# Kernel optimization log

Hardware: AMD Instinct MI355X
Metric: run time of the kernel (lower is better)

## Reference

```python
import jax, jax.numpy as jnp
import numpy as np

N = 128                      # mesh size (must be even)
IL_MMI = 0.05                # insersion_loss_MMI
IMB = 0.005                  # imbalance_MMI
IL_X = 0.02                  # insersion_loss_Crossing
CT = 0.01                    # cross_talk_Crossing
TWO_PI = 6.283185307179586


def _build_constants():
    aM = np.sqrt(1.0 - IL_MMI)
    # 2x2 MMI block (even pairing (0,1),(2,3),...)
    B_mmi = aM * np.array([[np.sqrt(0.5 + IMB), 1j * np.sqrt(0.5 - IMB)],
                           [1j * np.sqrt(0.5 - IMB), np.sqrt(0.5 + IMB)]], dtype=np.complex64)
    mmi_even = np.kron(np.eye(N, dtype=np.complex64), B_mmi)          # (2N, 2N)
    v_in = aM * np.array([[np.sqrt(0.5 + IMB)], [1j * np.sqrt(0.5 - IMB)]], dtype=np.complex64)
    mmi_in = np.kron(np.eye(N, dtype=np.complex64), v_in)             # (2N, N)
    w_out = aM * np.array([[np.sqrt(0.5 + IMB), 1j * np.sqrt(0.5 - IMB)]], dtype=np.complex64)
    mmi_out = np.kron(np.eye(N, dtype=np.complex64), w_out)           # (N, 2N)
    # crossing on 2N lines, blocks offset by 1, bar-state corners (N even branch)
    aX = np.sqrt(1.0 - IL_X)
    B_x = aX * np.array([[np.sqrt(CT), 1j * np.sqrt(1.0 - CT)],
                         [1j * np.sqrt(1.0 - CT), np.sqrt(CT)]], dtype=np.complex64)
    M = 2 * N
    cross = np.zeros((M, M), dtype=np.complex64)
    cross[0, 0] = aX * np.sqrt(1.0 - CT)
    cross[1:M - 1, 1:M - 1] = np.kron(np.eye((M - 2) // 2, dtype=np.complex64), B_x)
    cross[M - 1, M - 1] = aX * np.sqrt(1.0 - CT)
    return (jnp.asarray(mmi_in), jnp.asarray(mmi_even), jnp.asarray(cross), jnp.asarray(mmi_out))

MMI_IN, MMI_EVEN, CROSS, MMI_OUT = _build_constants()


def setup_inputs() -> dict:
    key = jax.random.key(0)
    k1, k2, k3 = jax.random.split(key, 3)
    theta_in = jax.random.uniform(k1, (N,), jnp.float32, 0.0, TWO_PI)
    theta_even = jax.random.uniform(k2, (2 * N - 1, N), jnp.float32, 0.0, TWO_PI)
    theta_out = jax.random.uniform(k3, (N,), jnp.float32, 0.0, TWO_PI)
    return {"theta_in": theta_in, "theta_even": theta_even, "theta_out": theta_out}


def reference(theta_in, theta_even, theta_out):
    # heater layers are diagonal -> apply as row scaling instead of matmul (same math)
    d_in = jnp.exp(1j * theta_in)                                      # (N,)
    d_ev = jnp.ones((2 * N - 1, 2 * N), jnp.complex64).at[:, ::2].set(jnp.exp(1j * theta_even))
    d_out = jnp.exp(1j * theta_out)                                    # (N,)

    # i == 0
    arch = d_in[:, None] * jnp.eye(N, dtype=jnp.complex64)             # ht_IN @ I
    arch = MMI_IN @ arch                                               # (2N, N)
    arch = CROSS @ (MMI_EVEN @ (d_ev[0][:, None] * arch))

    # i = 1 .. N-2 : (ht, MMI, ht, MMI, Crossing) per step
    da = d_ev[1:2 * N - 4:2]                                           # ht_even[2i-1], (N-2, 2N)
    db = d_ev[2:2 * N - 3:2]                                           # ht_even[2i],   (N-2, 2N)

    def step(arch, ds):
        a, b = ds
        arch = MMI_EVEN @ (a[:, None] * arch)
        arch = CROSS @ (MMI_EVEN @ (b[:, None] * arch))
        return arch, None

    arch, _ = jax.lax.scan(step, arch, (da, db))

    # i == N-1 : ht, MMI_even, ht, MMI_OUT, ht_OUT
    arch = MMI_EVEN @ (d_ev[2 * N - 3][:, None] * arch)
    arch = d_ev[2 * N - 2][:, None] * arch
    arch = MMI_OUT @ arch                                              # (N, N)
    arch = d_out[:, None] * arch
    return arch
```

## Files before the change

kernel.cpp:

```cpp
#include <hip/hip_runtime.h>

#define NN 128

__device__ __forceinline__ float wshl1(float x) {
    return __int_as_float(__builtin_amdgcn_update_dpp(
        __float_as_int(x), __float_as_int(x), 0x130, 0xf, 0xf, false));
}
__device__ __forceinline__ float wshr1(float x) {
    return __int_as_float(__builtin_amdgcn_update_dpp(
        __float_as_int(x), __float_as_int(x), 0x138, 0xf, 0xf, false));
}

__device__ __forceinline__ float4 make_cs(float2 th) {
    float s0, c0, s1, c1;
    __sincosf(th.x, &s0, &c0);
    __sincosf(th.y, &s1, &c1);
    return make_float4(c0, s0, c1, s1);
}

__global__ __launch_bounds__(64) void mesh_fused_kernel(
    const float* __restrict__ theta_in,
    const float* __restrict__ theta_even,
    const float* __restrict__ theta_out,
    float* __restrict__ out)
{
    const int c = blockIdx.x;
    const int l = threadIdx.x;

    const float A  = sqrtf(0.95f * 0.505f);
    const float B  = sqrtf(0.95f * 0.495f);
    const float C2 = sqrtf(0.98f * 0.01f);
    const float S2 = sqrtf(0.98f * 0.99f);

    const float ec0 = (l == 0)  ? S2 : C2, es0 = (l == 0)  ? 0.f : S2;
    const float ec3 = (l == 63) ? S2 : C2, es3 = (l == 63) ? 0.f : S2;

    const float2* TL = (const float2*)theta_even + l;
    float2 t0 = TL[0*64], t1 = TL[1*64], t2 = TL[2*64], t3 = TL[3*64],
           t4 = TL[4*64], t5 = TL[5*64], t6 = TL[6*64], t7 = TL[7*64];

    float2 v0 = make_float2(0.f, 0.f), v1 = v0, v2 = v0, v3 = v0;
    {
        float s, co;
        __sincosf(theta_in[c], &s, &co);
        float2 e0 = make_float2(A * co, A * s);
        float2 e1 = make_float2(-B * s, B * co);
        if (l == (c >> 1)) {
            if (c & 1) { v2 = e0; v3 = e1; }
            else       { v0 = e0; v1 = e1; }
        }
    }

    auto layer = [&](float4 t) {
        float rx = t.x * v0.x - t.y * v0.y;
        float ry = t.x * v0.y + t.y * v0.x;
        float qx = t.z * v2.x - t.w * v2.y;
        float qy = t.z * v2.y + t.w * v2.x;
        float2 n0, n1, n2, n3;
        n0.x = A * rx   - B * v1.y;  n0.y = A * ry   + B * v1.x;
        n1.x = A * v1.x - B * ry;    n1.y = A * v1.y + B * rx;
        n2.x = A * qx   - B * v3.y;  n2.y = A * qy   + B * v3.x;
        n3.x = A * v3.x - B * qy;    n3.y = A * v3.y + B * qx;
        v0 = n0; v1 = n1; v2 = n2; v3 = n3;
    };
    auto crossl = [&]() {
        float nx = wshl1(v0.x), ny = wshl1(v0.y);
        float px = wshr1(v3.x), py = wshr1(v3.y);
        float2 m0, m1, m2, m3;
        m0.x = ec0 * v0.x - es0 * py;  m0.y = ec0 * v0.y + es0 * px;
        m3.x = ec3 * v3.x - es3 * ny;  m3.y = ec3 * v3.y + es3 * nx;
        m1.x = C2 * v1.x - S2 * v2.y;  m1.y = C2 * v1.y + S2 * v2.x;
        m2.x = C2 * v2.x - S2 * v1.y;  m2.y = C2 * v2.y + S2 * v1.x;
        v0 = m0; v1 = m1; v2 = m2; v3 = m3;
    };

    float4 cf = make_cs(t0);

    for (int j8 = 0; j8 < 248; j8 += 8) {
        { t0 = TL[(j8+ 8)*64]; float4 cfn = make_cs(t1); layer(cf); crossl(); cf = cfn; }
        { t1 = TL[(j8+ 9)*64]; float4 cfn = make_cs(t2); layer(cf);           cf = cfn; }
        { t2 = TL[(j8+10)*64]; float4 cfn = make_cs(t3); layer(cf); crossl(); cf = cfn; }
        { t3 = TL[(j8+11)*64]; float4 cfn = make_cs(t4); layer(cf);           cf = cfn; }
        { t4 = TL[(j8+12)*64]; float4 cfn = make_cs(t5); layer(cf); crossl(); cf = cfn; }
        { t5 = TL[(j8+13)*64]; float4 cfn = make_cs(t6); layer(cf);           cf = cfn; }
        { t6 = TL[(j8+14)*64]; float4 cfn = make_cs(t7); layer(cf); crossl(); cf = cfn; }
        { int i7 = j8 + 15; if (i7 > 254) i7 = 254;
          t7 = TL[i7*64];      float4 cfn = make_cs(t0); layer(cf);           cf = cfn; }
    }
    { float4 cfn = make_cs(t1); layer(cf); crossl(); cf = cfn; }
    { float4 cfn = make_cs(t2); layer(cf);           cf = cfn; }
    { float4 cfn = make_cs(t3); layer(cf); crossl(); cf = cfn; }
    { float4 cfn = make_cs(t4); layer(cf);           cf = cfn; }
    { float4 cfn = make_cs(t5); layer(cf); crossl(); cf = cfn; }
    { float4 cfn = make_cs(t6); layer(cf);           cf = cfn; }

    float rx = cf.x * v0.x - cf.y * v0.y;
    float ry = cf.x * v0.y + cf.y * v0.x;
    float qx = cf.z * v2.x - cf.w * v2.y;
    float qy = cf.z * v2.y + cf.w * v2.x;
    float2 o0, o1;
    o0.x = A * rx - B * v1.y;  o0.y = A * ry + B * v1.x;
    o1.x = A * qx - B * v3.y;  o1.y = A * qy + B * v3.x;

    float2 tho = ((const float2*)theta_out)[l];
    float s0, c0, s1, c1;
    __sincosf(tho.x, &s0, &c0);
    __sincosf(tho.y, &s1, &c1);
    out[(2 * l)     * NN + c] = c0 * o0.x - s0 * o0.y;
    out[(2 * l + 1) * NN + c] = c1 * o1.x - s1 * o1.y;
}

extern "C" void kernel_launch(void* const* d_in, const int* in_sizes, int n_in,
                              void* d_out, int out_size, void* d_ws, size_t ws_size,
                              hipStream_t stream) {
    int ev = 0;
    for (int i = 0; i < n_in; ++i) if (in_sizes[i] > 1000) ev = i;
    int a = -1, b = -1;
    for (int i = 0; i < n_in; ++i) {
        if (i == ev) continue;
        if (a < 0) a = i; else if (b < 0) b = i;
    }
    const float* th_in  = (const float*)d_in[a];
    const float* th_ev  = (const float*)d_in[ev];
    const float* th_out = (const float*)d_in[b];
    mesh_fused_kernel<<<dim3(NN), dim3(64), 0, stream>>>(
        th_in, th_ev, th_out, (float*)d_out);
}
```

Baseline: 29.87 us.

## Split mesh propagation into two half-chains and combine via matrix product

Splits the 255-layer serial chain into two halves. 128 blocks propagate the input columns through the first half, and 256 blocks propagate unit basis vectors through the second half, giving a transfer matrix. A second kernel multiplies the two to form the output and applies the output phases. This halves the serial depth per block and uses more CUs, at the cost of a second kernel launch, extra global traffic through workspace, and a 256-term complex dot product per output.

```diff
diff --git a/kernel.cpp b/kernel.cpp
--- a/kernel.cpp
+++ b/kernel.cpp
@@ -18,38 +18,26 @@
     return make_float4(c0, s0, c1, s1);
 }
 
-__global__ __launch_bounds__(64) void mesh_fused_kernel(
-    const float* __restrict__ theta_in,
-    const float* __restrict__ theta_even,
-    const float* __restrict__ theta_out,
-    float* __restrict__ out)
-{
-    const int c = blockIdx.x;
-    const int l = threadIdx.x;
-
+__device__ __forceinline__ float2 cmuladd(float2 acc, float2 x, float2 y) {
+    acc.x += x.x * y.x - x.y * y.y;
+    acc.y += x.x * y.y + x.y * y.x;
+    return acc;
+}
+
+template<int J0>
+__device__ __forceinline__ float4 run127(const float2* __restrict__ TL, const int l,
+                                         float2& v0, float2& v1, float2& v2, float2& v3)
+{
     const float A  = sqrtf(0.95f * 0.505f);
     const float B  = sqrtf(0.95f * 0.495f);
     const float C2 = sqrtf(0.98f * 0.01f);
     const float S2 = sqrtf(0.98f * 0.99f);
-
     const float ec0 = (l == 0)  ? S2 : C2, es0 = (l == 0)  ? 0.f : S2;
     const float ec3 = (l == 63) ? S2 : C2, es3 = (l == 63) ? 0.f : S2;
 
-    const float2* TL = (const float2*)theta_even + l;
-    float2 t0 = TL[0*64], t1 = TL[1*64], t2 = TL[2*64], t3 = TL[3*64],
-           t4 = TL[4*64], t5 = TL[5*64], t6 = TL[6*64], t7 = TL[7*64];
-
-    float2 v0 = make_float2(0.f, 0.f), v1 = v0, v2 = v0, v3 = v0;
-    {
-        float s, co;
-        __sincosf(theta_in[c], &s, &co);
-        float2 e0 = make_float2(A * co, A * s);
-        float2 e1 = make_float2(-B * s, B * co);
-        if (l == (c >> 1)) {
-            if (c & 1) { v2 = e0; v3 = e1; }
-            else       { v0 = e0; v1 = e1; }
-        }
-    }
+    float2 t0 = TL[(J0+0)*64], t1 = TL[(J0+1)*64], t2 = TL[(J0+2)*64],
+           t3 = TL[(J0+3)*64], t4 = TL[(J0+4)*64], t5 = TL[(J0+5)*64],
+           t6 = TL[(J0+6)*64], t7 = TL[(J0+7)*64];
 
     auto layer = [&](float4 t) {
         float rx = t.x * v0.x - t.y * v0.y;
@@ -76,24 +64,126 @@
 
     float4 cf = make_cs(t0);
 
-    for (int j8 = 0; j8 < 248; j8 += 8) {
-        { t0 = TL[(j8+ 8)*64]; float4 cfn = make_cs(t1); layer(cf); crossl(); cf = cfn; }
-        { t1 = TL[(j8+ 9)*64]; float4 cfn = make_cs(t2); layer(cf);           cf = cfn; }
-        { t2 = TL[(j8+10)*64]; float4 cfn = make_cs(t3); layer(cf); crossl(); cf = cfn; }
-        { t3 = TL[(j8+11)*64]; float4 cfn = make_cs(t4); layer(cf);           cf = cfn; }
-        { t4 = TL[(j8+12)*64]; float4 cfn = make_cs(t5); layer(cf); crossl(); cf = cfn; }
-        { t5 = TL[(j8+13)*64]; float4 cfn = make_cs(t6); layer(cf);           cf = cfn; }
-        { t6 = TL[(j8+14)*64]; float4 cfn = make_cs(t7); layer(cf); crossl(); cf = cfn; }
-        { int i7 = j8 + 15; if (i7 > 254) i7 = 254;
-          t7 = TL[i7*64];      float4 cfn = make_cs(t0); layer(cf);           cf = cfn; }
-    }
-    { float4 cfn = make_cs(t1); layer(cf); crossl(); cf = cfn; }
-    { float4 cfn = make_cs(t2); layer(cf);           cf = cfn; }
-    { float4 cfn = make_cs(t3); layer(cf); crossl(); cf = cfn; }
-    { float4 cfn = make_cs(t4); layer(cf);           cf = cfn; }
-    { float4 cfn = make_cs(t5); layer(cf); crossl(); cf = cfn; }
-    { float4 cfn = make_cs(t6); layer(cf);           cf = cfn; }
-
+    for (int j8 = J0; j8 < J0 + 120; j8 += 8) {
+        { t0 = TL[(j8+ 8)*64]; float4 cfn = make_cs(t1); layer(cf); if (((J0+0)&1)==0) crossl(); cf = cfn; }
+        { t1 = TL[(j8+ 9)*64]; float4 cfn = make_cs(t2); layer(cf); if (((J0+1)&1)==0) crossl(); cf = cfn; }
+        { t2 = TL[(j8+10)*64]; float4 cfn = make_cs(t3); layer(cf); if (((J0+2)&1)==0) crossl(); cf = cfn; }
+        { t3 = TL[(j8+11)*64]; float4 cfn = make_cs(t4); layer(cf); if (((J0+3)&1)==0) crossl(); cf = cfn; }
+        { t4 = TL[(j8+12)*64]; float4 cfn = make_cs(t5); layer(cf); if (((J0+4)&1)==0) crossl(); cf = cfn; }
+        { t5 = TL[(j8+13)*64]; float4 cfn = make_cs(t6); layer(cf); if (((J0+5)&1)==0) crossl(); cf = cfn; }
+        { t6 = TL[(j8+14)*64]; float4 cfn = make_cs(t7); layer(cf); if (((J0+6)&1)==0) crossl(); cf = cfn; }
+        { t7 = TL[(j8+15)*64]; float4 cfn = make_cs(t0); layer(cf); if (((J0+7)&1)==0) crossl(); cf = cfn; }
+    }
+    { float4 cfn = make_cs(t1); layer(cf); if (((J0+0)&1)==0) crossl(); cf = cfn; }
+    { float4 cfn = make_cs(t2); layer(cf); if (((J0+1)&1)==0) crossl(); cf = cfn; }
+    { float4 cfn = make_cs(t3); layer(cf); if (((J0+2)&1)==0) crossl(); cf = cfn; }
+    { float4 cfn = make_cs(t4); layer(cf); if (((J0+3)&1)==0) crossl(); cf = cfn; }
+    { float4 cfn = make_cs(t5); layer(cf); if (((J0+4)&1)==0) crossl(); cf = cfn; }
+    { float4 cfn = make_cs(t6); layer(cf); if (((J0+5)&1)==0) crossl(); cf = cfn; }
+    { float4 cfn = make_cs(t7); layer(cf); if (((J0+6)&1)==0) crossl(); cf = cfn; }
+    return cf;
+}
+
+__global__ __launch_bounds__(64) void phase_kernel(
+    const float* __restrict__ theta_in,
+    const float* __restrict__ theta_even,
+    float2* __restrict__ M1T,
+    float2* __restrict__ T2T)
+{
+    const int bid = blockIdx.x;
+    const int l = threadIdx.x;
+    const float A = sqrtf(0.95f * 0.505f);
+    const float B = sqrtf(0.95f * 0.495f);
+    const float2* TL = (const float2*)theta_even + l;
+
+    float2 v0 = make_float2(0.f, 0.f), v1 = v0, v2 = v0, v3 = v0;
+
+    if (bid < 128) {
+        const int c = bid;
+        float s, co;
+        __sincosf(theta_in[c], &s, &co);
+        if (l == (c >> 1)) {
+            float2 e0 = make_float2(A * co, A * s);
+            float2 e1 = make_float2(-B * s, B * co);
+            if (c & 1) { v2 = e0; v3 = e1; }
+            else       { v0 = e0; v1 = e1; }
+        }
+        run127<0>(TL, l, v0, v1, v2, v3);
+        float4* dst = (float4*)(M1T + (size_t)c * 256 + 4 * l);
+        dst[0] = make_float4(v0.x, v0.y, v1.x, v1.y);
+        dst[1] = make_float4(v2.x, v2.y, v3.x, v3.y);
+    } else {
+        const int g = bid - 128;
+        if (l == (g >> 2)) {
+            float2 one = make_float2(1.f, 0.f);
+            int k = g & 3;
+            if      (k == 0) v0 = one;
+            else if (k == 1) v1 = one;
+            else if (k == 2) v2 = one;
+            else             v3 = one;
+        }
+        float4 cf = run127<127>(TL, l, v0, v1, v2, v3);
+        float rx = cf.x * v0.x - cf.y * v0.y;
+        float ry = cf.x * v0.y + cf.y * v0.x;
+        float qx = cf.z * v2.x - cf.w * v2.y;
+        float qy = cf.z * v2.y + cf.w * v2.x;
+        float4 o;
+        o.x = A * rx - B * v1.y;  o.y = A * ry + B * v1.x;
+        o.z = A * qx - B * v3.y;  o.w = A * qy + B * v3.x;
+        *(float4*)(T2T + (size_t)g * 128 + 2 * l) = o;
+    }
+}
+
+__global__ __launch_bounds__(64) void combine_kernel(
+    const float2* __restrict__ M1T,
+    const float2* __restrict__ T2T,
+    const float* __restrict__ theta_out,
+    float* __restrict__ out)
+{
+    const int c = blockIdx.x;
+    const int l = threadIdx.x;
+    const float2* m1 = M1T + (size_t)c * 256;
+
+    float2 acc0 = make_float2(0.f, 0.f), acc1 = acc0;
+    #pragma unroll 8
+    for (int g = 0; g < 256; ++g) {
+        float2 m = m1[g];
+        float4 t = *(const float4*)(T2T + (size_t)g * 128 + 2 * l);
+        acc0 = cmuladd(acc0, make_float2(t.x, t.y), m);
+        acc1 = cmuladd(acc1, make_float2(t.z, t.w), m);
+    }
+
+    float2 tho = ((const float2*)theta_out)[l];
+    float s0, c0, s1, c1;
+    __sincosf(tho.x, &s0, &c0);
+    __sincosf(tho.y, &s1, &c1);
+    out[(2 * l)     * NN + c] = c0 * acc0.x - s0 * acc0.y;
+    out[(2 * l + 1) * NN + c] = c1 * acc1.x - s1 * acc1.y;
+}
+
+__global__ __launch_bounds__(64) void mesh_fused_kernel(
+    const float* __restrict__ theta_in, const float* __restrict__ theta_even,
+    const float* __restrict__ theta_out, float* __restrict__ out)
+{
+    const int c = blockIdx.x;
+    const int l = threadIdx.x;
+    const float A = sqrtf(0.95f * 0.505f);
+    const float B = sqrtf(0.95f * 0.495f);
+    const float2* TL = (const float2*)theta_even + l;
+
+    float2 v0 = make_float2(0.f, 0.f), v1 = v0, v2 = v0, v3 = v0;
+    {
+        float s, co;
+        __sincosf(theta_in[c], &s, &co);
+        if (l == (c >> 1)) {
+            float2 e0 = make_float2(A * co, A * s);
+            float2 e1 = make_float2(-B * s, B * co);
+            if (c & 1) { v2 = e0; v3 = e1; }
+            else       { v0 = e0; v1 = e1; }
+        }
+    }
+    run127<0>(TL, l, v0, v1, v2, v3);
+    float4 cf = run127<127>(TL, l, v0, v1, v2, v3);
     float rx = cf.x * v0.x - cf.y * v0.y;
     float ry = cf.x * v0.y + cf.y * v0.x;
     float qx = cf.z * v2.x - cf.w * v2.y;
@@ -101,7 +191,6 @@
     float2 o0, o1;
     o0.x = A * rx - B * v1.y;  o0.y = A * ry + B * v1.x;
     o1.x = A * qx - B * v3.y;  o1.y = A * qy + B * v3.x;
-
     float2 tho = ((const float2*)theta_out)[l];
     float s0, c0, s1, c1;
     __sincosf(tho.x, &s0, &c0);
@@ -123,6 +212,15 @@
     const float* th_in  = (const float*)d_in[a];
     const float* th_ev  = (const float*)d_in[ev];
     const float* th_out = (const float*)d_in[b];
-    mesh_fused_kernel<<<dim3(NN), dim3(64), 0, stream>>>(
-        th_in, th_ev, th_out, (float*)d_out);
-}
+
+    const size_t m1_bytes = (size_t)128 * 256 * sizeof(float2);
+    const size_t t2_bytes = (size_t)256 * 128 * sizeof(float2);
+    if (ws_size >= m1_bytes + t2_bytes) {
+        float2* M1T = (float2*)d_ws;
+        float2* T2T = (float2*)((char*)d_ws + m1_bytes);
+        phase_kernel<<<dim3(384), dim3(64), 0, stream>>>(th_in, th_ev, M1T, T2T);
+        combine_kernel<<<dim3(128), dim3(64), 0, stream>>>(M1T, T2T, th_out, (float*)d_out);
+    } else {
+        mesh_fused_kernel<<<dim3(NN), dim3(64), 0, stream>>>(th_in, th_ev, th_out, (float*)d_out);
+    }
+}
```

Result: slower. 32.32 us (+8.2%).
